# Kernel tuning notes

Measured on AMD Instinct MI355X. Metric: run time of the kernel, lower is better.

The kernel has to match this reference:

```python
import jax, jax.numpy as jnp
import numpy as np

LN_EPS = 1e-5  # torch.nn.LayerNorm default


def setup_inputs() -> dict:
    key = jax.random.key(0)
    k1, k2 = jax.random.split(key)
    N, D_IN, D_OUT, G = 4096, 512, 512, 32
    x = jax.random.normal(k1, (N, D_IN), dtype=jnp.float32)
    ln_w = jnp.ones((D_IN,), dtype=jnp.float32)
    ln_b = jnp.zeros((D_IN,), dtype=jnp.float32)
    scale = 1.0 / (np.sqrt(D_IN) * np.sqrt(G))
    fouriercoeffs = jax.random.normal(k2, (2, D_OUT, D_IN, G), dtype=jnp.float32) * scale
    bias = jnp.zeros((1, D_OUT), dtype=jnp.float32)
    return {"x": x, "ln_w": ln_w, "ln_b": ln_b, "fouriercoeffs": fouriercoeffs, "bias": bias}


def reference(x, ln_w, ln_b, fouriercoeffs, bias):
    # LayerNorm over last dim
    mu = jnp.mean(x, axis=-1, keepdims=True)
    var = jnp.mean((x - mu) ** 2, axis=-1, keepdims=True)
    xn = (x - mu) * jax.lax.rsqrt(var + LN_EPS) * ln_w + ln_b
    G = fouriercoeffs.shape[-1]
    k = jnp.arange(1, G + 1, dtype=xn.dtype)           # [G]
    arg = xn[:, :, None] * k                            # [N, D_in, G]
    c = jnp.cos(arg)
    s = jnp.sin(arg)
    # contraction over (inputdim, gridsize) -> GEMM-shaped einsum
    y = jnp.einsum('big,oig->bo', c, fouriercoeffs[0])
    y = y + jnp.einsum('big,oig->bo', s, fouriercoeffs[1])
    y = y + bias
    return y
```

## Files before the change

kernel.cpp:

```cpp
#include <hip/hip_runtime.h>
#include <hip/hip_bf16.h>


#define N_ROWS 4096
#define D_IN   512
#define D_OUT  512
#define KT     16384
#define BM 256
#define BN 256
#define SPLITK 8
#define NT 64

typedef short short8 __attribute__((ext_vector_type(8)));
typedef float float4v __attribute__((ext_vector_type(4)));

__device__ inline unsigned int pack2bf(float a, float b) {
    __hip_bfloat162 h = __float22bfloat162_rn(make_float2(a, b));
    union { __hip_bfloat162 h; unsigned int u; } cv;
    cv.h = h;
    return cv.u;
}

__device__ inline unsigned short bf16_1(float a) {
    union { float f; unsigned int u; } cv;
    cv.f = a;
    unsigned int r = (cv.u + 0x7fff + ((cv.u >> 16) & 1)) >> 16;
    return (unsigned short)r;
}

__global__ __launch_bounds__(256) void pre_kernel(const float* __restrict__ x,
        const float* __restrict__ lnw, const float* __restrict__ lnb,
        const float* __restrict__ fc, float2* __restrict__ csT,
        unsigned short* __restrict__ Wb) {
    __shared__ __align__(16) float xs[16 * 516];
    __shared__ float2 murs[16];
    const int t = threadIdx.x;
    const int r0 = blockIdx.x * 16;
    {
        const int row = t >> 4, tq = t & 15;
        const float* xr = x + (size_t)(r0 + row) * D_IN;
        float s = 0.f, q = 0.f;
        #pragma unroll
        for (int k = 0; k < 8; ++k) {
            float4 v = *(const float4*)(xr + tq * 4 + k * 64);
            *(float4*)&xs[row * 516 + tq * 4 + k * 64] = v;
            s += v.x + v.y + v.z + v.w;
            q += v.x * v.x + v.y * v.y + v.z * v.z + v.w * v.w;
        }
        #pragma unroll
        for (int off = 8; off > 0; off >>= 1) {
            s += __shfl_xor(s, off, 16);
            q += __shfl_xor(q, off, 16);
        }
        if (tq == 0) {
            float mu = s * (1.f / D_IN);
            float var = q * (1.f / D_IN) - mu * mu;
            murs[row] = make_float2(mu, rsqrtf(var + 1e-5f));
        }
    }
    __syncthreads();
    {
        const int brow = t & 15, dimg = t >> 4;
        const float2 mr = murs[brow];
        #pragma unroll 4
        for (int j = 0; j < 32; ++j) {
            const int dim = j * 16 + dimg;
            float xv = xs[brow * 516 + dim];
            float xn = (xv - mr.x) * mr.y * lnw[dim] + lnb[dim];
            float s1, c1;
            __sincosf(xn, &s1, &c1);
            csT[(size_t)dim * N_ROWS + r0 + brow] = make_float2(c1, s1);
        }
    }
    {
        size_t e = ((size_t)blockIdx.x * 256 + t) * 8;
        for (int it2 = 0; it2 < 32; ++it2, e += (size_t)256 * 256 * 8) {
            const float4* in = (const float4*)(fc + e);
            float4 a = in[0], c = in[1];
            uint4 o;
            o.x = pack2bf(a.x, a.y);
            o.y = pack2bf(a.z, a.w);
            o.z = pack2bf(c.x, c.y);
            o.w = pack2bf(c.z, c.w);
            *(uint4*)(Wb + e) = o;
        }
    }
}

__device__ inline void stage_feats(unsigned short* Abuf, float2 cs, int ttype,
                                   int frow, int ihalf) {
    const float c1 = cs.x, s1 = cs.y;
    const float c2 = c1 + c1;
    float prev = ttype ? 0.f : 1.f;
    float cur  = ttype ? s1 : c1;
    const int rbase = frow * 64;
    const int sw = frow & 7;
    unsigned int us[4];
    #pragma unroll
    for (int d = 0; d < 16; ++d) {
        float f0 = cur;
        float f1 = __builtin_fmaf(c2, cur, -prev);
        float f2 = __builtin_fmaf(c2, f1, -cur);
        prev = f1;
        cur = f2;
        us[d & 3] = pack2bf(f0, f1);
        if ((d & 3) == 3) {
            const int kc = ihalf * 4 + (d >> 2);
            *(uint4*)&Abuf[rbase + ((kc ^ sw) << 3)] =
                make_uint4(us[0], us[1], us[2], us[3]);
        }
    }
}

__device__ inline void gl_lds16(const unsigned short* gsrc, unsigned short* ldst) {
    __builtin_amdgcn_global_load_lds(
        (const __attribute__((address_space(1))) unsigned int*)gsrc,
        (__attribute__((address_space(3))) unsigned int*)ldst, 16, 0, 0);
}

template<bool PF>
__device__ __forceinline__ void gemm_tile(int tt,
        const unsigned short* Ap, const unsigned short* Bp,
        unsigned short* Aw, unsigned short* Bw,
        const unsigned short* Bg0, const float2* csBase, float2& csA,
        int wv, int wrow, int lm, int lq, int swA, int bBase,
        int arow, int adim, float4v (&acc)[8][4]) {
    const int ttype1 = ((tt + 1) >> 5) & 1;
    const float c2 = csA.x + csA.x;
    float prev = ttype1 ? 0.f : 1.f;
    float cur  = ttype1 ? csA.y : csA.x;
    float2 csN = csA;
    short8 bf[4];
    #pragma unroll
    for (int p = 0; p < 4; ++p) {
        const int mh = p & 1, h = p >> 1;
        short8 af[4];
        #pragma unroll
        for (int j = 0; j < 4; ++j)
            af[j] = *(const short8*)
                &Ap[(wrow * 128 + (4 * mh + j) * 16 + lm) * 64
                    + (((h * 4 + lq) ^ swA) << 3)];
        if (p == 0 || p == 2) {
            #pragma unroll
            for (int n = 0; n < 4; ++n)
                bf[n] = *(const short8*)&Bp[bBase + n * 1024 + h * 256];
        }
        if (PF && p == 0) {
            const int n1 = tt + 1;
            const unsigned short* gb =
                Bg0 + (size_t)(n1 >> 5) * D_OUT * KT + (n1 & 31) * 64;
            unsigned short* ldst = Bw + (wv * 4) * 512;
            #pragma unroll
            for (int j2 = 0; j2 < 4; ++j2)
                gl_lds16(gb + (size_t)(j2 * 8) * KT, ldst + j2 * 512);
            __builtin_amdgcn_sched_barrier(0);
            csN = csBase[(size_t)(((tt + 2) & 31) * 2) * N_ROWS];
        }
        __builtin_amdgcn_s_barrier();
        asm volatile("s_waitcnt lgkmcnt(0)" ::: "memory");
        __builtin_amdgcn_s_setprio(1);
        #pragma unroll
        for (int j = 0; j < 4; ++j)
            #pragma unroll
            for (int n = 0; n < 4; ++n)
                acc[4 * mh + j][n] = __builtin_amdgcn_mfma_f32_16x16x32_bf16(
                    af[j], bf[n], acc[4 * mh + j][n], 0, 0, 0);
        __builtin_amdgcn_s_setprio(0);
        if (PF) {
            unsigned int us[4];
            #pragma unroll
            for (int d = 0; d < 4; ++d) {
                float f0 = cur;
                float f1 = __builtin_fmaf(c2, cur, -prev);
                us[d] = pack2bf(f0, f1);
                float f2 = __builtin_fmaf(c2, f1, -cur);
                prev = f1;
                cur = f2;
            }
            const int kc = adim * 4 + p;
            *(uint4*)&Aw[arow * 64 + ((kc ^ (arow & 7)) << 3)] =
                make_uint4(us[0], us[1], us[2], us[3]);
        }
        if (p < 3) {
            __builtin_amdgcn_s_barrier();
            asm volatile("" ::: "memory");
        } else if (PF) {
            asm volatile("s_waitcnt vmcnt(1) lgkmcnt(0)" ::: "memory");
            __builtin_amdgcn_s_barrier();
            asm volatile("" ::: "memory");
        }
    }
    if (PF) csA = csN;
}

__global__ __launch_bounds__(512, 2) void fkan_gemm(const float2* __restrict__ csT,
        const unsigned short* __restrict__ Wb, unsigned short* __restrict__ pb) {
    __shared__ unsigned short As[2][BM * 64];
    __shared__ unsigned short Bs[2][BN * 64];
    const int t = threadIdx.x;
    const int row0 = blockIdx.x * BM;
    const int col0 = blockIdx.y * BN;
    const int kz = blockIdx.z;
    const int k0 = kz * 2048;
    const int i0 = kz * 64;
    const int l = t & 63, wv = t >> 6;
    const int wrow = wv >> 2, wcol = wv & 3;
    const int lm = l & 15, lq = l >> 4;
    const int swA = lm & 7;
    const int arow = t & 255, adim = t >> 8;
    const int c8 = l & 7, s8 = l >> 3;
    const unsigned short* Bg0 =
        Wb + (size_t)(col0 + wv * 32 + c8) * KT + k0 + s8 * 8;
    const int bBase = (wcol * 8 + (lm >> 3)) * 512 + lq * 64 + (lm & 7) * 8;
    const float2* csBase = csT + (size_t)(i0 + adim) * N_ROWS + row0 + arow;

    float4v acc[8][4];
    #pragma unroll
    for (int i = 0; i < 8; ++i)
        #pragma unroll
        for (int j = 0; j < 4; ++j)
            acc[i][j] = (float4v){0.f, 0.f, 0.f, 0.f};

    float2 cs0 = csBase[0];
    #pragma unroll
    for (int j = 0; j < 4; ++j)
        gl_lds16(Bg0 + (size_t)(j * 8) * KT, &Bs[0][(wv * 4 + j) * 512]);
    __builtin_amdgcn_sched_barrier(0);
    float2 csA = csBase[2 * N_ROWS];
    stage_feats(&As[0][0], cs0, 0, arow, adim);
    asm volatile("s_waitcnt vmcnt(1) lgkmcnt(0)" ::: "memory");
    __builtin_amdgcn_s_barrier();
    asm volatile("" ::: "memory");

    #pragma unroll 1
    for (int tt = 0; tt < NT - 1; ++tt)
        gemm_tile<true>(tt, &As[tt & 1][0], &Bs[tt & 1][0],
                        &As[(tt + 1) & 1][0], &Bs[(tt + 1) & 1][0],
                        Bg0, csBase, csA, wv, wrow, lm, lq, swA, bBase,
                        arow, adim, acc);
    gemm_tile<false>(NT - 1, &As[1][0], &Bs[1][0], &As[0][0], &Bs[0][0],
                     Bg0, csBase, csA, wv, wrow, lm, lq, swA, bBase,
                     arow, adim, acc);

    unsigned short* pc = pb + (size_t)kz * N_ROWS * D_OUT;
    #pragma unroll
    for (int m = 0; m < 8; ++m)
        #pragma unroll
        for (int n = 0; n < 4; ++n)
            #pragma unroll
            for (int r = 0; r < 4; ++r) {
                const int row = row0 + wrow * 128 + m * 16 + lq * 4 + r;
                const int col = col0 + wcol * 64 + n * 16 + lm;
                pc[(size_t)row * D_OUT + col] = bf16_1(acc[m][n][r]);
            }
}

__global__ __launch_bounds__(256) void reduce_kernel(const unsigned short* __restrict__ pb,
        const float* __restrict__ bias, float* __restrict__ out) {
    const size_t e = ((size_t)blockIdx.x * 256 + threadIdx.x) * 8;
    const int col = (int)(e & (D_OUT - 1));
    float4 s0 = *(const float4*)(bias + col);
    float4 s1 = *(const float4*)(bias + col + 4);
    #pragma unroll
    for (int c = 0; c < SPLITK; ++c) {
        uint4 u = *(const uint4*)(pb + (size_t)c * N_ROWS * D_OUT + e);
        union { unsigned int u; float f; } lo, hi;
        lo.u = u.x << 16;            hi.u = u.x & 0xffff0000u;
        s0.x += lo.f;                s0.y += hi.f;
        lo.u = u.y << 16;            hi.u = u.y & 0xffff0000u;
        s0.z += lo.f;                s0.w += hi.f;
        lo.u = u.z << 16;            hi.u = u.z & 0xffff0000u;
        s1.x += lo.f;                s1.y += hi.f;
        lo.u = u.w << 16;            hi.u = u.w & 0xffff0000u;
        s1.z += lo.f;                s1.w += hi.f;
    }
    *(float4*)(out + e) = s0;
    *(float4*)(out + e + 4) = s1;
}

extern "C" void kernel_launch(void* const* d_in, const int* in_sizes, int n_in,
                              void* d_out, int out_size, void* d_ws, size_t ws_size,
                              hipStream_t stream) {
    const float* x    = (const float*)d_in[0];
    const float* ln_w = (const float*)d_in[1];
    const float* ln_b = (const float*)d_in[2];
    const float* fc   = (const float*)d_in[3];
    const float* bias = (const float*)d_in[4];
    float* out = (float*)d_out;

    float2* csT = (float2*)d_ws;
    unsigned short* Wb = (unsigned short*)((char*)d_ws + (16u << 20));
    unsigned short* pbp = (unsigned short*)((char*)d_ws + (48u << 20));

    pre_kernel<<<256, 256, 0, stream>>>(x, ln_w, ln_b, fc, csT, Wb);
    fkan_gemm<<<dim3(N_ROWS / BM, D_OUT / BN, SPLITK), 512, 0, stream>>>(csT, Wb, pbp);
    reduce_kernel<<<1024, 256, 0, stream>>>(pbp, bias, out);
}
```

Baseline: 256.9 us.

## Software-pipeline LDS reads ahead of MFMAs and remap block indices for locality

Restructures the inner tile loop so the LDS fragment reads for the next quarter are issued before the barrier and the current MFMA group, which also drops the s_waitcnt lgkmcnt(0) that used to sit right before each MFMA batch. The goal is to overlap LDS latency with matrix work. It also remaps the linear block id so that consecutive blocks share the same row tile across split-K and column combos, which should help L2 reuse of the weight and cos/sin data. Holding more fragments in flight raises register pressure under launch_bounds(512,2).

```diff
diff --git a/kernel.cpp b/kernel.cpp
--- a/kernel.cpp
+++ b/kernel.cpp
@@ -118,6 +118,9 @@
         (__attribute__((address_space(3))) unsigned int*)ldst, 16, 0, 0);
 }
 
+#define PACING_BAR() do { asm volatile("" ::: "memory"); \
+    __builtin_amdgcn_s_barrier(); asm volatile("" ::: "memory"); } while (0)
+
 template<bool PF>
 __device__ __forceinline__ void gemm_tile(int tt,
         const unsigned short* Ap, const unsigned short* Bp,
@@ -130,67 +133,76 @@
     float prev = ttype1 ? 0.f : 1.f;
     float cur  = ttype1 ? csA.y : csA.x;
     float2 csN = csA;
-    short8 bf[4];
-    #pragma unroll
-    for (int p = 0; p < 4; ++p) {
-        const int mh = p & 1, h = p >> 1;
-        short8 af[4];
-        #pragma unroll
-        for (int j = 0; j < 4; ++j)
-            af[j] = *(const short8*)
-                &Ap[(wrow * 128 + (4 * mh + j) * 16 + lm) * 64
-                    + (((h * 4 + lq) ^ swA) << 3)];
-        if (p == 0 || p == 2) {
-            #pragma unroll
-            for (int n = 0; n < 4; ++n)
-                bf[n] = *(const short8*)&Bp[bBase + n * 1024 + h * 256];
-        }
-        if (PF && p == 0) {
-            const int n1 = tt + 1;
-            const unsigned short* gb =
-                Bg0 + (size_t)(n1 >> 5) * D_OUT * KT + (n1 & 31) * 64;
-            unsigned short* ldst = Bw + (wv * 4) * 512;
-            #pragma unroll
-            for (int j2 = 0; j2 < 4; ++j2)
-                gl_lds16(gb + (size_t)(j2 * 8) * KT, ldst + j2 * 512);
-            __builtin_amdgcn_sched_barrier(0);
-            csN = csBase[(size_t)(((tt + 2) & 31) * 2) * N_ROWS];
-        }
+
+    #define A_RD(mh, j, h) (*(const short8*)\
+        &Ap[(wrow * 128 + (4 * (mh) + (j)) * 16 + lm) * 64 \
+            + ((((h) * 4 + lq) ^ swA) << 3)])
+    #define B_RD(n, h) (*(const short8*)&Bp[bBase + (n) * 1024 + (h) * 256])
+    #define MFMA16(AF, BF, mh) do { __builtin_amdgcn_s_setprio(1); \
+        _Pragma("unroll") for (int j = 0; j < 4; ++j) \
+            _Pragma("unroll") for (int n = 0; n < 4; ++n) \
+                acc[4 * (mh) + j][n] = __builtin_amdgcn_mfma_f32_16x16x32_bf16( \
+                    AF[j], BF[n], acc[4 * (mh) + j][n], 0, 0, 0); \
+        __builtin_amdgcn_s_setprio(0); } while (0)
+    #define STAGE_Q(q) do { unsigned int us[4]; \
+        _Pragma("unroll") for (int d = 0; d < 4; ++d) { \
+            float f0 = cur; \
+            float f1 = __builtin_fmaf(c2, cur, -prev); \
+            us[d] = pack2bf(f0, f1); \
+            float f2 = __builtin_fmaf(c2, f1, -cur); \
+            prev = f1; cur = f2; } \
+        const int kc = adim * 4 + (q); \
+        *(uint4*)&Aw[arow * 64 + ((kc ^ (arow & 7)) << 3)] = \
+            make_uint4(us[0], us[1], us[2], us[3]); } while (0)
+
+    short8 af0[4], bfA[4];
+    #pragma unroll
+    for (int j = 0; j < 4; ++j) af0[j] = A_RD(0, j, 0);
+    #pragma unroll
+    for (int n = 0; n < 4; ++n) bfA[n] = B_RD(n, 0);
+    MFMA16(af0, bfA, 0);
+    if (PF) {
+        const int n1 = tt + 1;
+        const unsigned short* gb =
+            Bg0 + (size_t)(n1 >> 5) * D_OUT * KT + (n1 & 31) * 64;
+        unsigned short* ldst = Bw + (wv * 4) * 512;
+        #pragma unroll
+        for (int j2 = 0; j2 < 4; ++j2)
+            gl_lds16(gb + (size_t)(j2 * 8) * KT, ldst + j2 * 512);
+        __builtin_amdgcn_sched_barrier(0);
+        csN = csBase[(size_t)(((tt + 2) & 31) * 2) * N_ROWS];
+    }
+    short8 af1[4];
+    #pragma unroll
+    for (int j = 0; j < 4; ++j) af1[j] = A_RD(1, j, 0);
+    if (PF) STAGE_Q(0);
+    PACING_BAR();
+    MFMA16(af1, bfA, 1);
+    short8 af2[4], bfB[4];
+    #pragma unroll
+    for (int j = 0; j < 4; ++j) af2[j] = A_RD(0, j, 1);
+    #pragma unroll
+    for (int n = 0; n < 4; ++n) bfB[n] = B_RD(n, 1);
+    if (PF) STAGE_Q(1);
+    PACING_BAR();
+    MFMA16(af2, bfB, 0);
+    short8 af3[4];
+    #pragma unroll
+    for (int j = 0; j < 4; ++j) af3[j] = A_RD(1, j, 1);
+    if (PF) STAGE_Q(2);
+    PACING_BAR();
+    MFMA16(af3, bfB, 1);
+    if (PF) {
+        STAGE_Q(3);
+        asm volatile("s_waitcnt vmcnt(1) lgkmcnt(0)" ::: "memory");
         __builtin_amdgcn_s_barrier();
-        asm volatile("s_waitcnt lgkmcnt(0)" ::: "memory");
-        __builtin_amdgcn_s_setprio(1);
-        #pragma unroll
-        for (int j = 0; j < 4; ++j)
-            #pragma unroll
-            for (int n = 0; n < 4; ++n)
-                acc[4 * mh + j][n] = __builtin_amdgcn_mfma_f32_16x16x32_bf16(
-                    af[j], bf[n], acc[4 * mh + j][n], 0, 0, 0);
-        __builtin_amdgcn_s_setprio(0);
-        if (PF) {
-            unsigned int us[4];
-            #pragma unroll
-            for (int d = 0; d < 4; ++d) {
-                float f0 = cur;
-                float f1 = __builtin_fmaf(c2, cur, -prev);
-                us[d] = pack2bf(f0, f1);
-                float f2 = __builtin_fmaf(c2, f1, -cur);
-                prev = f1;
-                cur = f2;
-            }
-            const int kc = adim * 4 + p;
-            *(uint4*)&Aw[arow * 64 + ((kc ^ (arow & 7)) << 3)] =
-                make_uint4(us[0], us[1], us[2], us[3]);
-        }
-        if (p < 3) {
-            __builtin_amdgcn_s_barrier();
-            asm volatile("" ::: "memory");
-        } else if (PF) {
-            asm volatile("s_waitcnt vmcnt(1) lgkmcnt(0)" ::: "memory");
-            __builtin_amdgcn_s_barrier();
-            asm volatile("" ::: "memory");
-        }
-    }
-    if (PF) csA = csN;
+        asm volatile("" ::: "memory");
+        csA = csN;
+    }
+    #undef A_RD
+    #undef B_RD
+    #undef MFMA16
+    #undef STAGE_Q
 }
 
 __global__ __launch_bounds__(512, 2) void fkan_gemm(const float2* __restrict__ csT,
@@ -198,9 +210,12 @@
     __shared__ unsigned short As[2][BM * 64];
     __shared__ unsigned short Bs[2][BN * 64];
     const int t = threadIdx.x;
-    const int row0 = blockIdx.x * BM;
-    const int col0 = blockIdx.y * BN;
-    const int kz = blockIdx.z;
+    const int lb = blockIdx.x + 16 * (blockIdx.y + 2 * blockIdx.z);
+    const int combo = (lb & 7) + 8 * (lb >> 7);
+    const int xrt = (lb >> 3) & 15;
+    const int row0 = xrt * BM;
+    const int col0 = (combo & 1) * BN;
+    const int kz = combo >> 1;
     const int k0 = kz * 2048;
     const int i0 = kz * 64;
     const int l = t & 63, wv = t >> 6;
```

After: 264.3 us. 2.9% more time.
